# Optimization experiments

Measured on AMD Instinct MI355X. Metric: run time of the kernel, lower is better.

Reference implementation:

```python
import jax, jax.numpy as jnp
import numpy as np

K = 3          # kernel_size
BOARD = 15     # gomoku board H = W
HOUT = BOARD - K + 1   # 13 windows per spatial dim
DIM_IN = 2 * K * K     # 18 binary features per window -> perfect hash


def fake_quant(x, scale, bits=8):
    """Straight-through fake quantization: round to int grid, clamp to bit range."""
    qmax = 2 ** (bits - 1) - 1
    y = jnp.clip(jnp.round(x * scale), -qmax - 1, qmax) / scale
    return x + jax.lax.stop_gradient(y - x)


def setup_inputs() -> dict:
    key = jax.random.key(0)
    ks = jax.random.split(key, 8)
    B = 8192
    board = jax.random.randint(ks[0], (B, 2, BOARD, BOARD), 0, 2, dtype=jnp.int32)
    emb = jax.random.normal(ks[1], (2 ** 18, 32), dtype=jnp.float32) * 0.05
    w1 = jax.random.normal(ks[2], (32, 32), dtype=jnp.float32) * 0.1
    b1 = jax.random.normal(ks[3], (32,), dtype=jnp.float32) * 0.05
    w2 = jax.random.normal(ks[4], (32, 32), dtype=jnp.float32) * 0.1
    b2 = jax.random.normal(ks[5], (32,), dtype=jnp.float32) * 0.05
    w3 = jax.random.normal(ks[6], (3, 32), dtype=jnp.float32) * 0.1
    b3 = jax.random.normal(ks[7], (3,), dtype=jnp.float32) * 0.05
    return {"board": board, "emb": emb, "w1": w1, "b1": b1,
            "w2": w2, "b2": b2, "w3": w3, "b3": b3}


def reference(board, emb, w1, b1, w2, b2, w3, b3):
    B = board.shape[0]
    # im2col unfold in torch F.unfold order (channel-major, then kernel row, col)
    # patches: (B, HOUT, HOUT, C*K*K)
    patches = jnp.stack(
        [board[:, c, i:i + HOUT, j:j + HOUT]
         for c in range(2) for i in range(K) for j in range(K)], axis=-1)
    # perfect hash of 18 binary features -> index into 2^18 embedding table
    powers = (2 ** jnp.arange(DIM_IN)).astype(jnp.int32)
    idx = jnp.sum(patches * powers, axis=-1)          # (B, HOUT, HOUT)
    feats = emb[idx]                                  # (B, HOUT, HOUT, 32) gather
    feats = fake_quant(jnp.clip(feats, -1.0, 127 / 128), 128.0, bits=8)
    v = jnp.sum(feats, axis=(1, 2))                   # (B, 32) clamp-sum accumulate
    # tiny quantized 3-layer value MLP
    for i, (wt, bs) in enumerate(((w1, b1), (w2, b2), (w3, b3))):
        v = jnp.clip(v, -1.0 if i == 0 else 0.0, 127 / 128)
        wq = fake_quant(wt, 128.0, bits=8)
        bq = fake_quant(bs, 128.0 * 128.0, bits=32)
        v = v @ wq.T + bq
    policy = jnp.zeros((B, BOARD, BOARD), dtype=v.dtype)
    return (v, policy)
```

## Files before the change

kernel.cpp:

```cpp
#include <hip/hip_runtime.h>
#include <stdint.h>

#define NW 169

typedef float f32x4 __attribute__((ext_vector_type(4)));

__device__ __forceinline__ float qw128(float x) {
    float r = rintf(x * 128.f);
    r = fminf(fmaxf(r, -128.f), 127.f);
    return r * 0.0078125f;
}
__device__ __forceinline__ float qb16384(float x) {
    return rintf(x * 16384.f) * 6.103515625e-05f;
}

__global__ void prep_kernel(const float* __restrict__ emb, uint8_t* __restrict__ q,
                            f32x4* __restrict__ policy) {
    int bid = blockIdx.x;
    int tid = threadIdx.x;
    if (bid >= 2048) {
        int i = (bid - 2048) * 256 + tid;
        f32x4 z = {0.f, 0.f, 0.f, 0.f};
        __builtin_nontemporal_store(z, &policy[i]);
        return;
    }
    int i = bid * 256 + tid;
    const float4* in4 = (const float4*)emb + (size_t)i * 4;
    uint32_t words[4];
#pragma unroll
    for (int t = 0; t < 4; ++t) {
        float4 f = in4[t];
        float v[4] = {f.x, f.y, f.z, f.w};
        uint32_t w = 0;
#pragma unroll
        for (int j = 0; j < 4; ++j) {
            float x = fminf(fmaxf(v[j], -1.f), 0.9921875f);
            int r = (int)rintf(x * 128.f) + 128;
            w |= ((uint32_t)r & 0xFFu) << (8 * j);
        }
        words[t] = w;
    }
    ((uint4*)q)[i] = make_uint4(words[0], words[1], words[2], words[3]);
}

__global__ __launch_bounds__(256)
void nnue_kernel(const int* __restrict__ board,
                 const uint8_t* __restrict__ embq,
                 const float* __restrict__ w1, const float* __restrict__ b1,
                 const float* __restrict__ w2, const float* __restrict__ b2,
                 const float* __restrict__ w3, const float* __restrict__ b3,
                 float* __restrict__ vout)
{
    __shared__ float w1T[32][32], w2T[32][32], w3T[32][4];
    __shared__ float b1q[32], b2q[32], b3q[4];
    __shared__ unsigned long long ballots[4][8];
    __shared__ int hashoff[4][192];
    __shared__ float vlds[4][32], h1lds[4][32], h2lds[4][32];

    int tid = threadIdx.x;
    for (int i = tid; i < 1024; i += 256) {
        int j = i & 31, k = i >> 5;
        w1T[k][j] = qw128(w1[j * 32 + k]);
        w2T[k][j] = qw128(w2[j * 32 + k]);
    }
    if (tid < 96) { int k = tid & 31, j = tid >> 5; w3T[k][j] = qw128(w3[j * 32 + k]); }
    if (tid < 32) { b1q[tid] = qb16384(b1[tid]); b2q[tid] = qb16384(b2[tid]); }
    if (tid < 3)  b3q[tid] = qb16384(b3[tid]);
    __syncthreads();

    int wv = tid >> 6, lane = tid & 63;
    int b = blockIdx.x * 4 + wv;
    const int* bp = board + b * 450;

#pragma unroll
    for (int t = 0; t < 8; ++t) {
        int n = t * 64 + lane;
        int cell = (n < 450) ? bp[n] : 0;
        unsigned long long m = __ballot(cell != 0);
        if (lane == 0) ballots[wv][t] = m;
    }

#pragma unroll
    for (int t = 0; t < 3; ++t) {
        int w = t * 64 + lane;
        int wi = w / 13;
        int wj = w - wi * 13;
        int idx = 0;
#pragma unroll
        for (int c = 0; c < 2; ++c) {
#pragma unroll
            for (int i = 0; i < 3; ++i) {
                int s = c * 225 + (min(wi, 12) + i) * 15;
                int word = s >> 6, off = s & 63;
                unsigned long long lo = ballots[wv][word];
                unsigned long long hi = ballots[wv][word + 1];
                unsigned long long bits = (lo >> off) | ((hi << 1) << (63 - off));
                idx |= (int)((bits >> wj) & 7ull) << (9 * c + 3 * i);
            }
        }
        hashoff[wv][w] = (w < NW) ? (idx << 5) : 0;
    }

    int d1 = lane & 1;
    int g = lane >> 1;
    const uint8_t* base = embq + d1 * 16;
    uint4 dv[6];
#pragma unroll
    for (int it = 0; it < 6; ++it) {
        int w = it * 32 + g;
        dv[it] = *(const uint4*)(base + hashoff[wv][w]);
    }
    const uint32_t M = 0x00FF00FFu;
    uint32_t a0lo = 0, a0hi = 0, a1lo = 0, a1hi = 0;
    uint32_t a2lo = 0, a2hi = 0, a3lo = 0, a3hi = 0;
#pragma unroll
    for (int it = 0; it < 6; ++it) {
        uint32_t x0 = dv[it].x, x1 = dv[it].y, x2 = dv[it].z, x3 = dv[it].w;
        if (it == 5) {
            uint32_t keep = (160 + g < NW) ? 0xFFFFFFFFu : 0u;
            x0 &= keep; x1 &= keep; x2 &= keep; x3 &= keep;
        }
        a0lo += x0 & M; a0hi += (x0 >> 8) & M;
        a1lo += x1 & M; a1hi += (x1 >> 8) & M;
        a2lo += x2 & M; a2hi += (x2 >> 8) & M;
        a3lo += x3 & M; a3hi += (x3 >> 8) & M;
    }
#pragma unroll
    for (int off = 2; off <= 32; off <<= 1) {
        a0lo += __shfl_xor(a0lo, off); a0hi += __shfl_xor(a0hi, off);
        a1lo += __shfl_xor(a1lo, off); a1hi += __shfl_xor(a1hi, off);
        a2lo += __shfl_xor(a2lo, off); a2hi += __shfl_xor(a2hi, off);
        a3lo += __shfl_xor(a3lo, off); a3hi += __shfl_xor(a3hi, off);
    }
    if (lane < 2) {
        uint32_t lo[4] = {a0lo, a1lo, a2lo, a3lo};
        uint32_t hi[4] = {a0hi, a1hi, a2hi, a3hi};
#pragma unroll
        for (int j = 0; j < 4; ++j) {
            int c[4];
            c[0] = (int)(lo[j] & 0xFFFFu) - 21632;
            c[1] = (int)(hi[j] & 0xFFFFu) - 21632;
            c[2] = (int)(lo[j] >> 16)     - 21632;
            c[3] = (int)(hi[j] >> 16)     - 21632;
#pragma unroll
            for (int u = 0; u < 4; ++u) {
                int cc = min(max(c[u], -128), 127);
                vlds[wv][d1 * 16 + j * 4 + u] = (float)cc * 0.0078125f;
            }
        }
    }

    int jj = lane & 31, hf = lane >> 5;
    float s1 = 0.f;
#pragma unroll
    for (int k2 = 0; k2 < 16; ++k2) {
        int k = hf * 16 + k2;
        s1 = fmaf(vlds[wv][k], w1T[k][jj], s1);
    }
    s1 += __shfl_xor(s1, 32);
    s1 += b1q[jj];
    s1 = fminf(fmaxf(s1, 0.f), 0.9921875f);
    if (lane < 32) h1lds[wv][jj] = s1;

    float s2 = 0.f;
#pragma unroll
    for (int k2 = 0; k2 < 16; ++k2) {
        int k = hf * 16 + k2;
        s2 = fmaf(h1lds[wv][k], w2T[k][jj], s2);
    }
    s2 += __shfl_xor(s2, 32);
    s2 += b2q[jj];
    s2 = fminf(fmaxf(s2, 0.f), 0.9921875f);
    if (lane < 32) h2lds[wv][jj] = s2;

    float s3 = 0.f;
    if (jj < 3) {
#pragma unroll
        for (int k2 = 0; k2 < 16; ++k2) {
            int k = hf * 16 + k2;
            s3 = fmaf(h2lds[wv][k], w3T[k][jj], s3);
        }
    }
    s3 += __shfl_xor(s3, 32);
    if (lane < 3) vout[b * 3 + lane] = s3 + b3q[lane];
}

extern "C" void kernel_launch(void* const* d_in, const int* in_sizes, int n_in,
                              void* d_out, int out_size, void* d_ws, size_t ws_size,
                              hipStream_t stream) {
    const int*   board = (const int*)d_in[0];
    const float* emb   = (const float*)d_in[1];
    const float* w1    = (const float*)d_in[2];
    const float* b1    = (const float*)d_in[3];
    const float* w2    = (const float*)d_in[4];
    const float* b2    = (const float*)d_in[5];
    const float* w3    = (const float*)d_in[6];
    const float* b3    = (const float*)d_in[7];
    float* out = (float*)d_out;
    uint8_t* embq = (uint8_t*)d_ws;

    prep_kernel<<<3848, 256, 0, stream>>>(emb, embq, (f32x4*)(out + 24576));
    nnue_kernel<<<2048, 256, 0, stream>>>(board, embq, w1, b1, w2, b2, w3, b3, out);
}
```

Measured before the change: 40.54 us.

## Process two boards per wave and halve grid to amortize weight setup

Each wave now handles two boards, issuing all twelve gather loads for both boards before reducing, and the grid shrinks to 1024 blocks. This halves the per-block cost of loading and quantizing the MLP weights into shared memory, and doubles the memory-level parallelism of the embedding gathers per wave. It also adds a launch_bounds occupancy hint and factors the quantize routine into a helper. The trade-off is higher register pressure from holding two sets of gathered vectors, and fewer blocks to spread across the GPU.

```diff
diff --git a/kernel.cpp b/kernel.cpp
--- a/kernel.cpp
+++ b/kernel.cpp
@@ -12,6 +12,26 @@
 }
 __device__ __forceinline__ float qb16384(float x) {
     return rintf(x * 16384.f) * 6.103515625e-05f;
+}
+
+__device__ __forceinline__ void quant_task(const float* __restrict__ emb,
+                                           uint8_t* __restrict__ q, int task) {
+    const float4* in4 = (const float4*)emb + (size_t)task * 4;
+    uint32_t words[4];
+#pragma unroll
+    for (int t = 0; t < 4; ++t) {
+        float4 f = in4[t];
+        float v[4] = {f.x, f.y, f.z, f.w};
+        uint32_t w = 0;
+#pragma unroll
+        for (int j = 0; j < 4; ++j) {
+            float x = fminf(fmaxf(v[j], -1.f), 0.9921875f);
+            int r = (int)rintf(x * 128.f) + 128;
+            w |= ((uint32_t)r & 0xFFu) << (8 * j);
+        }
+        words[t] = w;
+    }
+    ((uint4*)q)[task] = make_uint4(words[0], words[1], words[2], words[3]);
 }
 
 __global__ void prep_kernel(const float* __restrict__ emb, uint8_t* __restrict__ q,
@@ -24,26 +44,10 @@
         __builtin_nontemporal_store(z, &policy[i]);
         return;
     }
-    int i = bid * 256 + tid;
-    const float4* in4 = (const float4*)emb + (size_t)i * 4;
-    uint32_t words[4];
-#pragma unroll
-    for (int t = 0; t < 4; ++t) {
-        float4 f = in4[t];
-        float v[4] = {f.x, f.y, f.z, f.w};
-        uint32_t w = 0;
-#pragma unroll
-        for (int j = 0; j < 4; ++j) {
-            float x = fminf(fmaxf(v[j], -1.f), 0.9921875f);
-            int r = (int)rintf(x * 128.f) + 128;
-            w |= ((uint32_t)r & 0xFFu) << (8 * j);
-        }
-        words[t] = w;
-    }
-    ((uint4*)q)[i] = make_uint4(words[0], words[1], words[2], words[3]);
-}
-
-__global__ __launch_bounds__(256)
+    quant_task(emb, q, bid * 256 + tid);
+}
+
+__global__ __launch_bounds__(256, 4)
 void nnue_kernel(const int* __restrict__ board,
                  const uint8_t* __restrict__ embq,
                  const float* __restrict__ w1, const float* __restrict__ b1,
@@ -53,9 +57,9 @@
 {
     __shared__ float w1T[32][32], w2T[32][32], w3T[32][4];
     __shared__ float b1q[32], b2q[32], b3q[4];
-    __shared__ unsigned long long ballots[4][8];
-    __shared__ int hashoff[4][192];
-    __shared__ float vlds[4][32], h1lds[4][32], h2lds[4][32];
+    __shared__ unsigned long long ballots[8][8];
+    __shared__ int hashoff[8][192];
+    __shared__ float vlds[8][32], h1lds[8][32], h2lds[8][32];
 
     int tid = threadIdx.x;
     for (int i = tid; i < 1024; i += 256) {
@@ -69,120 +73,176 @@
     __syncthreads();
 
     int wv = tid >> 6, lane = tid & 63;
-    int b = blockIdx.x * 4 + wv;
-    const int* bp = board + b * 450;
-
-#pragma unroll
-    for (int t = 0; t < 8; ++t) {
-        int n = t * 64 + lane;
-        int cell = (n < 450) ? bp[n] : 0;
-        unsigned long long m = __ballot(cell != 0);
-        if (lane == 0) ballots[wv][t] = m;
-    }
-
-#pragma unroll
-    for (int t = 0; t < 3; ++t) {
-        int w = t * 64 + lane;
-        int wi = w / 13;
-        int wj = w - wi * 13;
-        int idx = 0;
-#pragma unroll
-        for (int c = 0; c < 2; ++c) {
-#pragma unroll
-            for (int i = 0; i < 3; ++i) {
-                int s = c * 225 + (min(wi, 12) + i) * 15;
-                int word = s >> 6, off = s & 63;
-                unsigned long long lo = ballots[wv][word];
-                unsigned long long hi = ballots[wv][word + 1];
-                unsigned long long bits = (lo >> off) | ((hi << 1) << (63 - off));
-                idx |= (int)((bits >> wj) & 7ull) << (9 * c + 3 * i);
+    int bbase = blockIdx.x * 8;
+    int sA = wv * 2, sB = wv * 2 + 1;
+
+#pragma unroll
+    for (int rb = 0; rb < 2; ++rb) {
+        int s = wv * 2 + rb;
+        const int* bp = board + (size_t)(bbase + s) * 450;
+#pragma unroll
+        for (int t = 0; t < 8; ++t) {
+            int n = t * 64 + lane;
+            int cell = (n < 450) ? bp[n] : 0;
+            unsigned long long m = __ballot(cell != 0);
+            if (lane == 0) ballots[s][t] = m;
+        }
+#pragma unroll
+        for (int t = 0; t < 3; ++t) {
+            int w = t * 64 + lane;
+            int wi = w / 13;
+            int wj = w - wi * 13;
+            int idx = 0;
+#pragma unroll
+            for (int c = 0; c < 2; ++c) {
+#pragma unroll
+                for (int i = 0; i < 3; ++i) {
+                    int st = c * 225 + (min(wi, 12) + i) * 15;
+                    int word = st >> 6, off = st & 63;
+                    unsigned long long lo = ballots[s][word];
+                    unsigned long long hi = ballots[s][word + 1];
+                    unsigned long long bits = (lo >> off) | ((hi << 1) << (63 - off));
+                    idx |= (int)((bits >> wj) & 7ull) << (9 * c + 3 * i);
+                }
             }
-        }
-        hashoff[wv][w] = (w < NW) ? (idx << 5) : 0;
+            hashoff[s][w] = (w < NW) ? (idx << 5) : 0;
+        }
     }
 
     int d1 = lane & 1;
     int g = lane >> 1;
     const uint8_t* base = embq + d1 * 16;
-    uint4 dv[6];
-#pragma unroll
-    for (int it = 0; it < 6; ++it) {
-        int w = it * 32 + g;
-        dv[it] = *(const uint4*)(base + hashoff[wv][w]);
-    }
+    uint4 dva[6], dvb[6];
+#pragma unroll
+    for (int it = 0; it < 6; ++it) dva[it] = *(const uint4*)(base + hashoff[sA][it * 32 + g]);
+#pragma unroll
+    for (int it = 0; it < 6; ++it) dvb[it] = *(const uint4*)(base + hashoff[sB][it * 32 + g]);
+
     const uint32_t M = 0x00FF00FFu;
-    uint32_t a0lo = 0, a0hi = 0, a1lo = 0, a1hi = 0;
-    uint32_t a2lo = 0, a2hi = 0, a3lo = 0, a3hi = 0;
-#pragma unroll
-    for (int it = 0; it < 6; ++it) {
-        uint32_t x0 = dv[it].x, x1 = dv[it].y, x2 = dv[it].z, x3 = dv[it].w;
-        if (it == 5) {
-            uint32_t keep = (160 + g < NW) ? 0xFFFFFFFFu : 0u;
-            x0 &= keep; x1 &= keep; x2 &= keep; x3 &= keep;
-        }
-        a0lo += x0 & M; a0hi += (x0 >> 8) & M;
-        a1lo += x1 & M; a1hi += (x1 >> 8) & M;
-        a2lo += x2 & M; a2hi += (x2 >> 8) & M;
-        a3lo += x3 & M; a3hi += (x3 >> 8) & M;
-    }
-#pragma unroll
-    for (int off = 2; off <= 32; off <<= 1) {
-        a0lo += __shfl_xor(a0lo, off); a0hi += __shfl_xor(a0hi, off);
-        a1lo += __shfl_xor(a1lo, off); a1hi += __shfl_xor(a1hi, off);
-        a2lo += __shfl_xor(a2lo, off); a2hi += __shfl_xor(a2hi, off);
-        a3lo += __shfl_xor(a3lo, off); a3hi += __shfl_xor(a3hi, off);
-    }
-    if (lane < 2) {
-        uint32_t lo[4] = {a0lo, a1lo, a2lo, a3lo};
-        uint32_t hi[4] = {a0hi, a1hi, a2hi, a3hi};
-#pragma unroll
-        for (int j = 0; j < 4; ++j) {
-            int c[4];
-            c[0] = (int)(lo[j] & 0xFFFFu) - 21632;
-            c[1] = (int)(hi[j] & 0xFFFFu) - 21632;
-            c[2] = (int)(lo[j] >> 16)     - 21632;
-            c[3] = (int)(hi[j] >> 16)     - 21632;
-#pragma unroll
-            for (int u = 0; u < 4; ++u) {
-                int cc = min(max(c[u], -128), 127);
-                vlds[wv][d1 * 16 + j * 4 + u] = (float)cc * 0.0078125f;
+    uint32_t keep5 = (160 + g < NW) ? 0xFFFFFFFFu : 0u;
+    int jj = lane & 31, hf = lane >> 5;
+
+    {
+        uint32_t a0lo = 0, a0hi = 0, a1lo = 0, a1hi = 0;
+        uint32_t a2lo = 0, a2hi = 0, a3lo = 0, a3hi = 0;
+#pragma unroll
+        for (int it = 0; it < 6; ++it) {
+            uint32_t x0 = dva[it].x, x1 = dva[it].y, x2 = dva[it].z, x3 = dva[it].w;
+            if (it == 5) { x0 &= keep5; x1 &= keep5; x2 &= keep5; x3 &= keep5; }
+            a0lo += x0 & M; a0hi += (x0 >> 8) & M;
+            a1lo += x1 & M; a1hi += (x1 >> 8) & M;
+            a2lo += x2 & M; a2hi += (x2 >> 8) & M;
+            a3lo += x3 & M; a3hi += (x3 >> 8) & M;
+        }
+#pragma unroll
+        for (int off = 2; off <= 32; off <<= 1) {
+            a0lo += __shfl_xor(a0lo, off); a0hi += __shfl_xor(a0hi, off);
+            a1lo += __shfl_xor(a1lo, off); a1hi += __shfl_xor(a1hi, off);
+            a2lo += __shfl_xor(a2lo, off); a2hi += __shfl_xor(a2hi, off);
+            a3lo += __shfl_xor(a3lo, off); a3hi += __shfl_xor(a3hi, off);
+        }
+        if (lane < 2) {
+            uint32_t lo[4] = {a0lo, a1lo, a2lo, a3lo};
+            uint32_t hi[4] = {a0hi, a1hi, a2hi, a3hi};
+#pragma unroll
+            for (int j = 0; j < 4; ++j) {
+                int c[4];
+                c[0] = (int)(lo[j] & 0xFFFFu) - 21632;
+                c[1] = (int)(hi[j] & 0xFFFFu) - 21632;
+                c[2] = (int)(lo[j] >> 16)     - 21632;
+                c[3] = (int)(hi[j] >> 16)     - 21632;
+#pragma unroll
+                for (int u = 0; u < 4; ++u) {
+                    int cc = min(max(c[u], -128), 127);
+                    vlds[sA][d1 * 16 + j * 4 + u] = (float)cc * 0.0078125f;
+                }
             }
         }
-    }
-
-    int jj = lane & 31, hf = lane >> 5;
-    float s1 = 0.f;
-#pragma unroll
-    for (int k2 = 0; k2 < 16; ++k2) {
-        int k = hf * 16 + k2;
-        s1 = fmaf(vlds[wv][k], w1T[k][jj], s1);
-    }
-    s1 += __shfl_xor(s1, 32);
-    s1 += b1q[jj];
-    s1 = fminf(fmaxf(s1, 0.f), 0.9921875f);
-    if (lane < 32) h1lds[wv][jj] = s1;
-
-    float s2 = 0.f;
-#pragma unroll
-    for (int k2 = 0; k2 < 16; ++k2) {
-        int k = hf * 16 + k2;
-        s2 = fmaf(h1lds[wv][k], w2T[k][jj], s2);
-    }
-    s2 += __shfl_xor(s2, 32);
-    s2 += b2q[jj];
-    s2 = fminf(fmaxf(s2, 0.f), 0.9921875f);
-    if (lane < 32) h2lds[wv][jj] = s2;
-
-    float s3 = 0.f;
-    if (jj < 3) {
-#pragma unroll
-        for (int k2 = 0; k2 < 16; ++k2) {
-            int k = hf * 16 + k2;
-            s3 = fmaf(h2lds[wv][k], w3T[k][jj], s3);
-        }
-    }
-    s3 += __shfl_xor(s3, 32);
-    if (lane < 3) vout[b * 3 + lane] = s3 + b3q[lane];
+        float t1 = 0.f;
+#pragma unroll
+        for (int k2 = 0; k2 < 16; ++k2) { int k = hf * 16 + k2; t1 = fmaf(vlds[sA][k], w1T[k][jj], t1); }
+        t1 += __shfl_xor(t1, 32);
+        t1 += b1q[jj];
+        t1 = fminf(fmaxf(t1, 0.f), 0.9921875f);
+        if (lane < 32) h1lds[sA][jj] = t1;
+
+        float t2 = 0.f;
+#pragma unroll
+        for (int k2 = 0; k2 < 16; ++k2) { int k = hf * 16 + k2; t2 = fmaf(h1lds[sA][k], w2T[k][jj], t2); }
+        t2 += __shfl_xor(t2, 32);
+        t2 += b2q[jj];
+        t2 = fminf(fmaxf(t2, 0.f), 0.9921875f);
+        if (lane < 32) h2lds[sA][jj] = t2;
+
+        float t3 = 0.f;
+        if (jj < 3) {
+#pragma unroll
+            for (int k2 = 0; k2 < 16; ++k2) { int k = hf * 16 + k2; t3 = fmaf(h2lds[sA][k], w3T[k][jj], t3); }
+        }
+        t3 += __shfl_xor(t3, 32);
+        if (lane < 3) vout[(size_t)(bbase + sA) * 3 + lane] = t3 + b3q[lane];
+    }
+
+    {
+        uint32_t a0lo = 0, a0hi = 0, a1lo = 0, a1hi = 0;
+        uint32_t a2lo = 0, a2hi = 0, a3lo = 0, a3hi = 0;
+#pragma unroll
+        for (int it = 0; it < 6; ++it) {
+            uint32_t x0 = dvb[it].x, x1 = dvb[it].y, x2 = dvb[it].z, x3 = dvb[it].w;
+            if (it == 5) { x0 &= keep5; x1 &= keep5; x2 &= keep5; x3 &= keep5; }
+            a0lo += x0 & M; a0hi += (x0 >> 8) & M;
+            a1lo += x1 & M; a1hi += (x1 >> 8) & M;
+            a2lo += x2 & M; a2hi += (x2 >> 8) & M;
+            a3lo += x3 & M; a3hi += (x3 >> 8) & M;
+        }
+#pragma unroll
+        for (int off = 2; off <= 32; off <<= 1) {
+            a0lo += __shfl_xor(a0lo, off); a0hi += __shfl_xor(a0hi, off);
+            a1lo += __shfl_xor(a1lo, off); a1hi += __shfl_xor(a1hi, off);
+            a2lo += __shfl_xor(a2lo, off); a2hi += __shfl_xor(a2hi, off);
+            a3lo += __shfl_xor(a3lo, off); a3hi += __shfl_xor(a3hi, off);
+        }
+        if (lane < 2) {
+            uint32_t lo[4] = {a0lo, a1lo, a2lo, a3lo};
+            uint32_t hi[4] = {a0hi, a1hi, a2hi, a3hi};
+#pragma unroll
+            for (int j = 0; j < 4; ++j) {
+                int c[4];
+                c[0] = (int)(lo[j] & 0xFFFFu) - 21632;
+                c[1] = (int)(hi[j] & 0xFFFFu) - 21632;
+                c[2] = (int)(lo[j] >> 16)     - 21632;
+                c[3] = (int)(hi[j] >> 16)     - 21632;
+#pragma unroll
+                for (int u = 0; u < 4; ++u) {
+                    int cc = min(max(c[u], -128), 127);
+                    vlds[sB][d1 * 16 + j * 4 + u] = (float)cc * 0.0078125f;
+                }
+            }
+        }
+        float t1 = 0.f;
+#pragma unroll
+        for (int k2 = 0; k2 < 16; ++k2) { int k = hf * 16 + k2; t1 = fmaf(vlds[sB][k], w1T[k][jj], t1); }
+        t1 += __shfl_xor(t1, 32);
+        t1 += b1q[jj];
+        t1 = fminf(fmaxf(t1, 0.f), 0.9921875f);
+        if (lane < 32) h1lds[sB][jj] = t1;
+
+        float t2 = 0.f;
+#pragma unroll
+        for (int k2 = 0; k2 < 16; ++k2) { int k = hf * 16 + k2; t2 = fmaf(h1lds[sB][k], w2T[k][jj], t2); }
+        t2 += __shfl_xor(t2, 32);
+        t2 += b2q[jj];
+        t2 = fminf(fmaxf(t2, 0.f), 0.9921875f);
+        if (lane < 32) h2lds[sB][jj] = t2;
+
+        float t3 = 0.f;
+        if (jj < 3) {
+#pragma unroll
+            for (int k2 = 0; k2 < 16; ++k2) { int k = hf * 16 + k2; t3 = fmaf(h2lds[sB][k], w3T[k][jj], t3); }
+        }
+        t3 += __shfl_xor(t3, 32);
+        if (lane < 3) vout[(size_t)(bbase + sB) * 3 + lane] = t3 + b3q[lane];
+    }
 }
 
 extern "C" void kernel_launch(void* const* d_in, const int* in_sizes, int n_in,
@@ -200,5 +260,5 @@
     uint8_t* embq = (uint8_t*)d_ws;
 
     prep_kernel<<<3848, 256, 0, stream>>>(emb, embq, (f32x4*)(out + 24576));
-    nnue_kernel<<<2048, 256, 0, stream>>>(board, embq, w1, b1, w2, b2, w3, b3, out);
-}
+    nnue_kernel<<<1024, 256, 0, stream>>>(board, embq, w1, b1, w2, b2, w3, b3, out);
+}
```

After: 40.91 us. Within noise of the previous version (+0.9%).
